# Kernel optimization log

Measured on AMD Instinct MI355X. Metric: run time of the kernel, lower is better.

Reference implementation:

```python
import jax, jax.numpy as jnp
import numpy as np

B, T, N, D = 16, 12, 512, 128
H, DH = 4, 32            # heads, per-head dim (out_dim = H*DH = 128)
E = 4096                  # edges in the static road graph
NEG_SLOPE = 0.2
LN_EPS = 1e-5


def setup_inputs() -> dict:
    key = jax.random.key(0)
    ks = jax.random.split(key, 9)
    x = jax.random.normal(ks[0], (B, T, N, D), dtype=jnp.float32)
    edge_index = jax.random.randint(ks[1], (2, E), 0, N, dtype=jnp.int64)
    edge_weight = jax.random.uniform(ks[2], (E,), dtype=jnp.float32)
    # GAT parameters (dropout in eval mode -> identity)
    W = jax.random.normal(ks[3], (D, H * DH), dtype=jnp.float32) * (1.0 / np.sqrt(D))
    att_src = jax.random.normal(ks[4], (H, DH), dtype=jnp.float32) * 0.1
    att_dst = jax.random.normal(ks[5], (H, DH), dtype=jnp.float32) * 0.1
    bias = jnp.zeros((H * DH,), dtype=jnp.float32)
    ln_gamma = jnp.ones((H * DH,), dtype=jnp.float32)
    ln_beta = jnp.zeros((H * DH,), dtype=jnp.float32)
    return {"x": x, "edge_index": edge_index, "edge_weight": edge_weight,
            "W": W, "att_src": att_src, "att_dst": att_dst, "bias": bias,
            "ln_gamma": ln_gamma, "ln_beta": ln_beta}


def reference(x, edge_index, edge_weight, W, att_src, att_dst, bias, ln_gamma, ln_beta):
    b, t, n, din = x.shape
    bt = b * t
    h_heads, dh = att_src.shape
    src, dst = edge_index[0], edge_index[1]

    # project: [BT, N, H, DH]
    h = (x.reshape(bt, n, din) @ W).reshape(bt, n, h_heads, dh)

    # per-node attention scores, then gather to edges: [BT, E, H]
    s_src = jnp.einsum('bnhd,hd->bnh', h, att_src)
    s_dst = jnp.einsum('bnhd,hd->bnh', h, att_dst)
    e = jax.nn.leaky_relu(s_src[:, src] + s_dst[:, dst], NEG_SLOPE)
    e = e * edge_weight[None, :, None]  # edge_weight modulates attention logits

    # scatter-softmax over incoming edges per destination node
    m = jnp.full((bt, n, h_heads), -1e30, dtype=e.dtype).at[:, dst].max(e)
    ex = jnp.exp(e - m[:, dst])
    denom = jnp.zeros((bt, n, h_heads), dtype=e.dtype).at[:, dst].add(ex)
    alpha = ex / (denom[:, dst] + 1e-16)  # [BT, E, H]

    # weighted aggregation (scatter-add) of source features
    msg = alpha[..., None] * h[:, src]  # [BT, E, H, DH]
    agg = jnp.zeros((bt, n, h_heads, dh), dtype=h.dtype).at[:, dst].add(msg)

    out = agg.reshape(b, t, n, h_heads * dh) + bias

    # LayerNorm then ELU
    mu = out.mean(axis=-1, keepdims=True)
    var = out.var(axis=-1, keepdims=True)
    out = (out - mu) * jax.lax.rsqrt(var + LN_EPS) * ln_gamma + ln_beta
    return jnp.where(out > 0, out, jnp.expm1(out))
```

## Files before the change

kernel.cpp:

```cpp
#include <hip/hip_runtime.h>

#define BT    192
#define NNODE 512
#define DIM   128
#define NH    4
#define DH    32
#define NE    4096
#define NROWS (BT * NNODE)
#define GEMM_BLOCKS (NROWS / 128)

typedef __attribute__((ext_vector_type(8))) short  short8b;
typedef __attribute__((ext_vector_type(4))) float  floatx4;
typedef __attribute__((ext_vector_type(8))) unsigned short ushort8;

__device__ inline unsigned short f2bf(float f) {
    unsigned int u = __float_as_uint(f);
    return (unsigned short)((u + 0x7FFFu + ((u >> 16) & 1u)) >> 16);
}
__device__ inline float bflo(unsigned int v) { return __uint_as_float(v << 16); }
__device__ inline float bfhi(unsigned int v) { return __uint_as_float(v & 0xFFFF0000u); }

__device__ inline short8b pack8(float4 a, float4 b) {
    short8b r;
    r[0] = (short)f2bf(a.x); r[1] = (short)f2bf(a.y);
    r[2] = (short)f2bf(a.z); r[3] = (short)f2bf(a.w);
    r[4] = (short)f2bf(b.x); r[5] = (short)f2bf(b.y);
    r[6] = (short)f2bf(b.z); r[7] = (short)f2bf(b.w);
    return r;
}

__global__ __launch_bounds__(512) void wswz_k(
    const float* __restrict__ W, unsigned short* __restrict__ wswz)
{
    int j = blockIdx.x * 512 + threadIdx.x;
    const float4* W4 = (const float4*)W;
    float4 wv = W4[j];
    int k = j >> 5, c4 = (j & 31) * 4;
    float vv[4] = { wv.x, wv.y, wv.z, wv.w };
#pragma unroll
    for (int e = 0; e < 4; ++e) {
        int col = c4 + e;
        int byte = col * 256 + ((2 * k) ^ ((col & 7) << 4));
        wswz[byte >> 1] = f2bf(vv[e]);
    }
}

__global__ __launch_bounds__(256) void gemm_mfma_k(
    const float* __restrict__ x, const unsigned short* __restrict__ wswz,
    const float* __restrict__ att_src, const float* __restrict__ att_dst,
    unsigned short* __restrict__ h, float* __restrict__ ssg,
    float* __restrict__ sdg,
    const int* __restrict__ ei, const float* __restrict__ ew,
    int* __restrict__ rp2, int* __restrict__ cs2,
    float* __restrict__ ce2, int* __restrict__ perm)
{
    __shared__ __align__(16) char sm[64 * 132 * 4];
    __shared__ float att_f[256];
    int t = threadIdx.x;

    if (blockIdx.x >= GEMM_BLOCKS) {
        int* dsts   = (int*)sm;
        int* cnt    = (int*)(sm + 16384);
        int* scn    = (int*)(sm + 18432);
        int* nodeAt = (int*)(sm + 20480);
        int* hist   = (int*)(sm + 22528);
        int* hscan  = (int*)(sm + 23552);
        int cb = blockIdx.x - GEMM_BLOCKS;
        int i0 = t, i1 = t + 256;

        for (int e = t; e < NE; e += 256) dsts[e] = ei[NE + e];
        cnt[i0] = 0; cnt[i1] = 0;
        hist[t] = 0;
        __syncthreads();
        for (int e = t; e < NE; e += 256) atomicAdd(&cnt[dsts[e]], 1);
        __syncthreads();

        int deg0 = cnt[i0], deg1 = cnt[i1];
        int b0 = (deg0 < 255) ? deg0 : 255;
        int b1 = (deg1 < 255) ? deg1 : 255;
        atomicAdd(&hist[b0], 1);
        atomicAdd(&hist[b1], 1);
        __syncthreads();
        hscan[t] = hist[t];
        __syncthreads();
        for (int o = 1; o < 256; o <<= 1) {
            int v = (t >= o) ? hscan[t - o] : 0;
            __syncthreads();
            hscan[t] += v;
            __syncthreads();
        }
        int off0 = 0, off1 = 0;
        for (int n = 0; n < i0; ++n) {
            int dn = cnt[n]; dn = (dn < 255) ? dn : 255;
            off0 += (dn == b0) ? 1 : 0;
        }
        for (int n = 0; n < i1; ++n) {
            int dn = cnt[n]; dn = (dn < 255) ? dn : 255;
            off1 += (dn == b1) ? 1 : 0;
        }
        int rank0 = hscan[b0] - hist[b0] + off0;
        int rank1 = hscan[b1] - hist[b1] + off1;
        nodeAt[rank0] = i0;
        nodeAt[rank1] = i1;
        __syncthreads();

        scn[i0] = cnt[nodeAt[i0]];
        scn[i1] = cnt[nodeAt[i1]];
        __syncthreads();
        for (int o = 1; o < NNODE; o <<= 1) {
            int v0 = (i0 >= o) ? scn[i0 - o] : 0;
            int v1 = (i1 >= o) ? scn[i1 - o] : 0;
            __syncthreads();
            scn[i0] += v0; scn[i1] += v1;
            __syncthreads();
        }
        if (cb == 0) {
            if (t == 0) rp2[0] = 0;
            rp2[i0 + 1] = scn[i0];
            rp2[i1 + 1] = scn[i1];
            perm[i0] = nodeAt[i0];
            perm[i1] = nodeAt[i1];
        }
        __syncthreads();

        int wave = t >> 6, lane = t & 63;
#pragma unroll
        for (int rr = 0; rr < 2; ++rr) {
            int r = cb * 8 + rr * 4 + wave;
            int node = nodeAt[r];
            int pos = scn[r] - cnt[node];
            for (int c = 0; c < NE; c += 64) {
                int e = c + lane;
                int d = dsts[e];
                unsigned long long mask = __ballot(d == node);
                if (d == node) {
                    int ofs = __popcll(mask & ((1ull << lane) - 1ull));
                    cs2[pos + ofs] = ei[e];
                    ce2[pos + ofs] = ew[e];
                }
                pos += __popcll(mask);
            }
        }
        return;
    }

    if (t < 128) att_f[t] = att_src[(t & 3) * 32 + (t >> 2)];
    else         att_f[t] = att_dst[(t & 3) * 32 + ((t - 128) >> 2)];
    {
        const uint4* g = (const uint4*)wswz;
        uint4* ld = (uint4*)sm;
#pragma unroll
        for (int i = 0; i < 8; ++i) ld[t + i * 256] = g[t + i * 256];
    }
    int w = t >> 6, l = t & 63, lr = l & 15, lk = l >> 4;
    size_t base = (size_t)blockIdx.x * 128;
    const float* xA = x + (base + (size_t)w * 16 + lr) * DIM;
    const float* xB = xA + 64 * DIM;

    floatx4 accA[8], accB[8];
#pragma unroll
    for (int n = 0; n < 8; ++n) {
        accA[n] = (floatx4){0.f, 0.f, 0.f, 0.f};
        accB[n] = (floatx4){0.f, 0.f, 0.f, 0.f};
    }
    __syncthreads();

#pragma unroll
    for (int kk = 0; kk < 4; ++kk) {
        int k0 = kk * 32 + lk * 8;
        float4 a0 = *(const float4*)(xA + k0);
        float4 a1 = *(const float4*)(xA + k0 + 4);
        float4 b0 = *(const float4*)(xB + k0);
        float4 b1 = *(const float4*)(xB + k0 + 4);
        short8b av = pack8(a0, a1);
        short8b bv = pack8(b0, b1);
        int c = kk * 4 + lk;
#pragma unroll
        for (int n = 0; n < 8; ++n) {
            int col = n * 16 + lr;
            short8b bf = *(const short8b*)(sm + col * 256 + ((c ^ (col & 7)) << 4));
            accA[n] = __builtin_amdgcn_mfma_f32_16x16x32_bf16(av, bf, accA[n], 0, 0, 0);
            accB[n] = __builtin_amdgcn_mfma_f32_16x16x32_bf16(bv, bf, accB[n], 0, 0, 0);
        }
    }

    float* Ct = (float*)sm;
    unsigned short* hbase = h + base * DIM;
    int sr = t >> 2, sq = t & 3;

    __syncthreads();
#pragma unroll
    for (int n = 0; n < 8; ++n)
#pragma unroll
        for (int j = 0; j < 4; ++j)
            Ct[(w * 16 + lk * 4 + j) * 132 + n * 16 + lr] = accA[n][j];
    __syncthreads();
#pragma unroll
    for (int i = 0; i < 4; ++i) {
        int chunk = t + i * 256;
        int row = chunk >> 4, cc = chunk & 15;
        const float* cp = Ct + row * 132 + cc * 8;
        ushort8 v;
#pragma unroll
        for (int e = 0; e < 8; ++e) v[e] = f2bf(cp[e]);
        *(ushort8*)(hbase + row * DIM + cc * 8) = v;
    }
    {
        const float* cp = Ct + sr * 132 + sq * 32;
        float ps = 0.f, pd = 0.f;
#pragma unroll
        for (int j = 0; j < 32; j += 4) {
            float4 cv = *(const float4*)(cp + j);
            ps = fmaf(cv.x, att_f[(j+0)*4 + sq], ps);
            ps = fmaf(cv.y, att_f[(j+1)*4 + sq], ps);
            ps = fmaf(cv.z, att_f[(j+2)*4 + sq], ps);
            ps = fmaf(cv.w, att_f[(j+3)*4 + sq], ps);
            pd = fmaf(cv.x, att_f[128 + (j+0)*4 + sq], pd);
            pd = fmaf(cv.y, att_f[128 + (j+1)*4 + sq], pd);
            pd = fmaf(cv.z, att_f[128 + (j+2)*4 + sq], pd);
            pd = fmaf(cv.w, att_f[128 + (j+3)*4 + sq], pd);
        }
        size_t grow = base + sr;
        ssg[grow * 4 + sq] = ps;
        sdg[grow * 4 + sq] = pd;
    }

    __syncthreads();
#pragma unroll
    for (int n = 0; n < 8; ++n)
#pragma unroll
        for (int j = 0; j < 4; ++j)
            Ct[(w * 16 + lk * 4 + j) * 132 + n * 16 + lr] = accB[n][j];
    __syncthreads();
#pragma unroll
    for (int i = 0; i < 4; ++i) {
        int chunk = t + i * 256;
        int row = chunk >> 4, cc = chunk & 15;
        const float* cp = Ct + row * 132 + cc * 8;
        ushort8 v;
#pragma unroll
        for (int e = 0; e < 8; ++e) v[e] = f2bf(cp[e]);
        *(ushort8*)(hbase + (64 + row) * DIM + cc * 8) = v;
    }
    {
        const float* cp = Ct + sr * 132 + sq * 32;
        float ps = 0.f, pd = 0.f;
#pragma unroll
        for (int j = 0; j < 32; j += 4) {
            float4 cv = *(const float4*)(cp + j);
            ps = fmaf(cv.x, att_f[(j+0)*4 + sq], ps);
            ps = fmaf(cv.y, att_f[(j+1)*4 + sq], ps);
            ps = fmaf(cv.z, att_f[(j+2)*4 + sq], ps);
            ps = fmaf(cv.w, att_f[(j+3)*4 + sq], ps);
            pd = fmaf(cv.x, att_f[128 + (j+0)*4 + sq], pd);
            pd = fmaf(cv.y, att_f[128 + (j+1)*4 + sq], pd);
            pd = fmaf(cv.z, att_f[128 + (j+2)*4 + sq], pd);
            pd = fmaf(cv.w, att_f[128 + (j+3)*4 + sq], pd);
        }
        size_t grow = base + 64 + sr;
        ssg[grow * 4 + sq] = ps;
        sdg[grow * 4 + sq] = pd;
    }
}

__global__ __launch_bounds__(1024) void agg_ln_k(
    const unsigned short* __restrict__ h,
    const float* __restrict__ ssg, const float* __restrict__ sdg,
    const int* __restrict__ rp2, const int* __restrict__ cs2,
    const float* __restrict__ ce2, const int* __restrict__ perm,
    const float* __restrict__ bias, const float* __restrict__ gamma,
    const float* __restrict__ beta, float* __restrict__ out)
{
    __shared__ unsigned int hs[NH][NNODE * 16];
    __shared__ float ssl[NNODE * NH];
    __shared__ float prm[384];
    int t  = threadIdx.x;
    int bt = blockIdx.x;

    const uint4* hg = (const uint4*)(h + (size_t)bt * NNODE * DIM);
    for (int i = t; i < NNODE * 16; i += 1024) {
        int n = i >> 4, c = i & 15, hh = c >> 2, j = c & 3;
        uint4 v = hg[i];
        int js = j ^ ((n >> 1) & 3);
        *(uint4*)&hs[hh][n * 16 + js * 4] = v;
    }
    const float* ssgb = ssg + (size_t)bt * NNODE * NH;
    for (int i = t; i < NNODE * NH; i += 1024) ssl[i] = ssgb[i];
    if (t < 384) prm[t] = (t < 128) ? bias[t] : (t < 256) ? gamma[t - 128] : beta[t - 256];
    __syncthreads();

    int l  = t & 63, w = t >> 6;
    int hh = l >> 4, rl = l & 15;
    int g  = w * 16 + rl;
    const float* sdgb = sdg + (size_t)bt * NNODE * NH;
    float* outb = out + (size_t)bt * NNODE * DIM;

#pragma unroll
    for (int pi = 0; pi < 2; ++pi) {
        int rank = pi ? (511 - g) : g;
        int node = perm[rank];
        int beg = rp2[rank], end = rp2[rank + 1];
        float sd = sdgb[node * 4 + hh];

        float acc[32];
#pragma unroll
        for (int d = 0; d < 32; ++d) acc[d] = 0.f;
        float den = 0.f;

        int e = beg;
        for (; e + 2 <= end; e += 2) {
            int   s0 = cs2[e],   s1 = cs2[e + 1];
            float w0 = ce2[e],   w1 = ce2[e + 1];
            float a0 = ssl[s0 * 4 + hh] + sd; a0 = (a0 > 0.f) ? a0 : 0.2f * a0;
            float a1 = ssl[s1 * 4 + hh] + sd; a1 = (a1 > 0.f) ? a1 : 0.2f * a1;
            float p0 = __expf(a0 * w0);
            float p1 = __expf(a1 * w1);
            den += p0; den += p1;
            const unsigned int* r0 = &hs[hh][s0 * 16];
            const unsigned int* r1 = &hs[hh][s1 * 16];
            int sx0 = (s0 >> 1) & 3, sx1 = (s1 >> 1) & 3;
#pragma unroll
            for (int j = 0; j < 4; ++j) {
                uint4 v0 = *(const uint4*)&r0[(j ^ sx0) * 4];
                uint4 v1 = *(const uint4*)&r1[(j ^ sx1) * 4];
                int d0 = j * 8;
                acc[d0+0] = fmaf(p0, bflo(v0.x), acc[d0+0]);
                acc[d0+1] = fmaf(p0, bfhi(v0.x), acc[d0+1]);
                acc[d0+2] = fmaf(p0, bflo(v0.y), acc[d0+2]);
                acc[d0+3] = fmaf(p0, bfhi(v0.y), acc[d0+3]);
                acc[d0+4] = fmaf(p0, bflo(v0.z), acc[d0+4]);
                acc[d0+5] = fmaf(p0, bfhi(v0.z), acc[d0+5]);
                acc[d0+6] = fmaf(p0, bflo(v0.w), acc[d0+6]);
                acc[d0+7] = fmaf(p0, bfhi(v0.w), acc[d0+7]);
                acc[d0+0] = fmaf(p1, bflo(v1.x), acc[d0+0]);
                acc[d0+1] = fmaf(p1, bfhi(v1.x), acc[d0+1]);
                acc[d0+2] = fmaf(p1, bflo(v1.y), acc[d0+2]);
                acc[d0+3] = fmaf(p1, bfhi(v1.y), acc[d0+3]);
                acc[d0+4] = fmaf(p1, bflo(v1.z), acc[d0+4]);
                acc[d0+5] = fmaf(p1, bfhi(v1.z), acc[d0+5]);
                acc[d0+6] = fmaf(p1, bflo(v1.w), acc[d0+6]);
                acc[d0+7] = fmaf(p1, bfhi(v1.w), acc[d0+7]);
            }
        }
        if (e < end) {
            int   s0 = cs2[e];
            float w0 = ce2[e];
            float a0 = ssl[s0 * 4 + hh] + sd; a0 = (a0 > 0.f) ? a0 : 0.2f * a0;
            float p0 = __expf(a0 * w0);
            den += p0;
            const unsigned int* r0 = &hs[hh][s0 * 16];
            int sx0 = (s0 >> 1) & 3;
#pragma unroll
            for (int j = 0; j < 4; ++j) {
                uint4 v0 = *(const uint4*)&r0[(j ^ sx0) * 4];
                int d0 = j * 8;
                acc[d0+0] = fmaf(p0, bflo(v0.x), acc[d0+0]);
                acc[d0+1] = fmaf(p0, bfhi(v0.x), acc[d0+1]);
                acc[d0+2] = fmaf(p0, bflo(v0.y), acc[d0+2]);
                acc[d0+3] = fmaf(p0, bfhi(v0.y), acc[d0+3]);
                acc[d0+4] = fmaf(p0, bflo(v0.z), acc[d0+4]);
                acc[d0+5] = fmaf(p0, bfhi(v0.z), acc[d0+5]);
                acc[d0+6] = fmaf(p0, bflo(v0.w), acc[d0+6]);
                acc[d0+7] = fmaf(p0, bfhi(v0.w), acc[d0+7]);
            }
        }

        float inv = 1.f / (den + 1e-16f);
        float s1 = 0.f, s2 = 0.f;
#pragma unroll
        for (int d = 0; d < 32; ++d) {
            float vv = fmaf(acc[d], inv, prm[hh * 32 + d]);
            acc[d] = vv;
            s1 += vv;
            s2 = fmaf(vv, vv, s2);
        }
        s1 += __shfl_xor(s1, 16, 64);
        s2 += __shfl_xor(s2, 16, 64);
        s1 += __shfl_xor(s1, 32, 64);
        s2 += __shfl_xor(s2, 32, 64);
        float mean = s1 * (1.f / 128.f);
        float var  = s2 * (1.f / 128.f) - mean * mean;
        float rstd = rsqrtf(var + 1e-5f);

        float* op = outb + (size_t)node * DIM + hh * 32;
#pragma unroll
        for (int d = 0; d < 32; d += 4) {
            int pd0 = 128 + hh * 32 + d, pb0 = 256 + hh * 32 + d;
            float y0 = (acc[d+0] - mean) * rstd * prm[pd0+0] + prm[pb0+0];
            float y1 = (acc[d+1] - mean) * rstd * prm[pd0+1] + prm[pb0+1];
            float y2 = (acc[d+2] - mean) * rstd * prm[pd0+2] + prm[pb0+2];
            float y3 = (acc[d+3] - mean) * rstd * prm[pd0+3] + prm[pb0+3];
            float4 o4;
            o4.x = (y0 > 0.f) ? y0 : expm1f(y0);
            o4.y = (y1 > 0.f) ? y1 : expm1f(y1);
            o4.z = (y2 > 0.f) ? y2 : expm1f(y2);
            o4.w = (y3 > 0.f) ? y3 : expm1f(y3);
            *(float4*)(op + d) = o4;
        }
    }
}

extern "C" void kernel_launch(void* const* d_in, const int* in_sizes, int n_in,
                              void* d_out, int out_size, void* d_ws, size_t ws_size,
                              hipStream_t stream)
{
    const float* x     = (const float*)d_in[0];
    const int*   ei    = (const int*)  d_in[1];
    const float* ew    = (const float*)d_in[2];
    const float* W     = (const float*)d_in[3];
    const float* asrc  = (const float*)d_in[4];
    const float* adst  = (const float*)d_in[5];
    const float* bias  = (const float*)d_in[6];
    const float* gamma = (const float*)d_in[7];
    const float* beta  = (const float*)d_in[8];
    float* out = (float*)d_out;

    char* ws = (char*)d_ws;
    unsigned short* h = (unsigned short*)ws;
    size_t off = (size_t)NROWS * DIM * sizeof(unsigned short);
    unsigned short* wswz = (unsigned short*)(ws + off);
    off += (size_t)DIM * DIM * sizeof(unsigned short);
    float* ssg = (float*)(ws + off);
    off += (size_t)NROWS * NH * sizeof(float);
    float* sdg = (float*)(ws + off);
    off += (size_t)NROWS * NH * sizeof(float);
    int* rp2 = (int*)(ws + off);
    off += (((NNODE + 1) * sizeof(int)) + 15) & ~(size_t)15;
    int* perm = (int*)(ws + off);
    off += (size_t)NNODE * sizeof(int);
    int* cs2 = (int*)(ws + off);
    off += (size_t)NE * sizeof(int);
    float* ce2 = (float*)(ws + off);
    off += (size_t)NE * sizeof(float);

    wswz_k<<<8, 512, 0, stream>>>(W, wswz);
    gemm_mfma_k<<<GEMM_BLOCKS + 64, 256, 0, stream>>>(
        x, wswz, asrc, adst, h, ssg, sdg, ei, ew, rp2, cs2, ce2, perm);
    agg_ln_k<<<BT, 1024, 0, stream>>>(h, ssg, sdg, rp2, cs2, ce2, perm,
                                      bias, gamma, beta, out);
}
```

Baseline: 70.73 us.

## Precompute normalized edge softmax weights into shared memory before aggregation

```diff
diff --git a/kernel.cpp b/kernel.cpp
--- a/kernel.cpp
+++ b/kernel.cpp
@@ -16,6 +16,9 @@
 __device__ inline unsigned short f2bf(float f) {
     unsigned int u = __float_as_uint(f);
     return (unsigned short)((u + 0x7FFFu + ((u >> 16) & 1u)) >> 16);
+}
+__device__ inline float bf2f(unsigned short s) {
+    return __uint_as_float(((unsigned int)s) << 16);
 }
 __device__ inline float bflo(unsigned int v) { return __uint_as_float(v << 16); }
 __device__ inline float bfhi(unsigned int v) { return __uint_as_float(v & 0xFFFF0000u); }
@@ -271,29 +274,22 @@
     const float* __restrict__ bias, const float* __restrict__ gamma,
     const float* __restrict__ beta, float* __restrict__ out)
 {
-    __shared__ unsigned int hs[NH][NNODE * 16];
-    __shared__ float ssl[NNODE * NH];
-    __shared__ float prm[384];
+    __shared__ __align__(16) unsigned char smem[131072 + 32768];
+    unsigned int*   hsbase = (unsigned int*)smem;
+    float*          ssl    = (float*)smem;
+    unsigned short* pbuf   = (unsigned short*)(smem + 131072);
+
     int t  = threadIdx.x;
     int bt = blockIdx.x;
-
-    const uint4* hg = (const uint4*)(h + (size_t)bt * NNODE * DIM);
-    for (int i = t; i < NNODE * 16; i += 1024) {
-        int n = i >> 4, c = i & 15, hh = c >> 2, j = c & 3;
-        uint4 v = hg[i];
-        int js = j ^ ((n >> 1) & 3);
-        *(uint4*)&hs[hh][n * 16 + js * 4] = v;
-    }
-    const float* ssgb = ssg + (size_t)bt * NNODE * NH;
-    for (int i = t; i < NNODE * NH; i += 1024) ssl[i] = ssgb[i];
-    if (t < 384) prm[t] = (t < 128) ? bias[t] : (t < 256) ? gamma[t - 128] : beta[t - 256];
-    __syncthreads();
 
     int l  = t & 63, w = t >> 6;
     int hh = l >> 4, rl = l & 15;
     int g  = w * 16 + rl;
+
+    const float* ssgb = ssg + (size_t)bt * NNODE * NH;
+    for (int i = t; i < NNODE * NH; i += 1024) ssl[i] = ssgb[i];
     const float* sdgb = sdg + (size_t)bt * NNODE * NH;
-    float* outb = out + (size_t)bt * NNODE * DIM;
+    __syncthreads();
 
 #pragma unroll
     for (int pi = 0; pi < 2; ++pi) {
@@ -301,23 +297,55 @@
         int node = perm[rank];
         int beg = rp2[rank], end = rp2[rank + 1];
         float sd = sdgb[node * 4 + hh];
+        float den = 0.f;
+        for (int e = beg; e < end; ++e) {
+            float a = ssl[cs2[e] * 4 + hh] + sd;
+            a = (a > 0.f) ? a : 0.2f * a;
+            float p = __expf(a * ce2[e]);
+            unsigned short pb = f2bf(p);
+            den += bf2f(pb);
+            pbuf[e * 4 + hh] = pb;
+        }
+        float inv = 1.f / (den + 1e-16f);
+        for (int e = beg; e < end; ++e) {
+            int idx = e * 4 + hh;
+            pbuf[idx] = f2bf(bf2f(pbuf[idx]) * inv);
+        }
+    }
+    __syncthreads();
+
+    const uint4* hg = (const uint4*)(h + (size_t)bt * NNODE * DIM);
+    for (int i = t; i < NNODE * 16; i += 1024) {
+        int n = i >> 4, c = i & 15, ch = c >> 2, j = c & 3;
+        uint4 v = hg[i];
+        int js = j ^ ((n >> 1) & 3);
+        *(uint4*)&hsbase[(size_t)ch * (NNODE * 16) + n * 16 + js * 4] = v;
+    }
+    __syncthreads();
+
+    const unsigned int* hsh = hsbase + (size_t)hh * (NNODE * 16);
+    float* outb = out + (size_t)bt * NNODE * DIM;
+    const float* bi = bias  + hh * 32;
+    const float* ga = gamma + hh * 32;
+    const float* be = beta  + hh * 32;
+
+#pragma unroll
+    for (int pi = 0; pi < 2; ++pi) {
+        int rank = pi ? (511 - g) : g;
+        int node = perm[rank];
+        int beg = rp2[rank], end = rp2[rank + 1];
 
         float acc[32];
 #pragma unroll
         for (int d = 0; d < 32; ++d) acc[d] = 0.f;
-        float den = 0.f;
 
         int e = beg;
         for (; e + 2 <= end; e += 2) {
             int   s0 = cs2[e],   s1 = cs2[e + 1];
-            float w0 = ce2[e],   w1 = ce2[e + 1];
-            float a0 = ssl[s0 * 4 + hh] + sd; a0 = (a0 > 0.f) ? a0 : 0.2f * a0;
-            float a1 = ssl[s1 * 4 + hh] + sd; a1 = (a1 > 0.f) ? a1 : 0.2f * a1;
-            float p0 = __expf(a0 * w0);
-            float p1 = __expf(a1 * w1);
-            den += p0; den += p1;
-            const unsigned int* r0 = &hs[hh][s0 * 16];
-            const unsigned int* r1 = &hs[hh][s1 * 16];
+            float p0 = bf2f(pbuf[e * 4 + hh]);
+            float p1 = bf2f(pbuf[(e + 1) * 4 + hh]);
+            const unsigned int* r0 = &hsh[s0 * 16];
+            const unsigned int* r1 = &hsh[s1 * 16];
             int sx0 = (s0 >> 1) & 3, sx1 = (s1 >> 1) & 3;
 #pragma unroll
             for (int j = 0; j < 4; ++j) {
@@ -344,11 +372,8 @@
         }
         if (e < end) {
             int   s0 = cs2[e];
-            float w0 = ce2[e];
-            float a0 = ssl[s0 * 4 + hh] + sd; a0 = (a0 > 0.f) ? a0 : 0.2f * a0;
-            float p0 = __expf(a0 * w0);
-            den += p0;
-            const unsigned int* r0 = &hs[hh][s0 * 16];
+            float p0 = bf2f(pbuf[e * 4 + hh]);
+            const unsigned int* r0 = &hsh[s0 * 16];
             int sx0 = (s0 >> 1) & 3;
 #pragma unroll
             for (int j = 0; j < 4; ++j) {
@@ -365,11 +390,10 @@
             }
         }
 
-        float inv = 1.f / (den + 1e-16f);
         float s1 = 0.f, s2 = 0.f;
 #pragma unroll
         for (int d = 0; d < 32; ++d) {
-            float vv = fmaf(acc[d], inv, prm[hh * 32 + d]);
+            float vv = acc[d] + bi[d];
             acc[d] = vv;
             s1 += vv;
             s2 = fmaf(vv, vv, s2);
@@ -385,11 +409,10 @@
         float* op = outb + (size_t)node * DIM + hh * 32;
 #pragma unroll
         for (int d = 0; d < 32; d += 4) {
-            int pd0 = 128 + hh * 32 + d, pb0 = 256 + hh * 32 + d;
-            float y0 = (acc[d+0] - mean) * rstd * prm[pd0+0] + prm[pb0+0];
-            float y1 = (acc[d+1] - mean) * rstd * prm[pd0+1] + prm[pb0+1];
-            float y2 = (acc[d+2] - mean) * rstd * prm[pd0+2] + prm[pb0+2];
-            float y3 = (acc[d+3] - mean) * rstd * prm[pd0+3] + prm[pb0+3];
+            float y0 = (acc[d+0] - mean) * rstd * ga[d+0] + be[d+0];
+            float y1 = (acc[d+1] - mean) * rstd * ga[d+1] + be[d+1];
+            float y2 = (acc[d+2] - mean) * rstd * ga[d+2] + be[d+2];
+            float y3 = (acc[d+3] - mean) * rstd * ga[d+3] + be[d+3];
             float4 o4;
             o4.x = (y0 > 0.f) ? y0 : expm1f(y0);
             o4.y = (y1 > 0.f) ? y1 : expm1f(y1);
```

New measurement: 81.54 us. 1.15x slower.
